# Kernel optimization log

Measured on AMD Instinct MI355X. Metric: run time of the kernel, lower is better.

## Reference

```python
import jax, jax.numpy as jnp
import numpy as np

EPS = 1e-5

def _layernorm(x, g, b):
    m = jnp.mean(x, axis=-1, keepdims=True)
    v = jnp.var(x, axis=-1, keepdims=True)
    return (x - m) * jax.lax.rsqrt(v + EPS) * g + b

def setup_inputs() -> dict:
    key = jax.random.key(0)
    ks = jax.random.split(key, 8)
    B, N, D, H = 4, 2048, 1024, 16
    F = 2 * D
    s = 0.02
    return {
        "x": jax.random.normal(ks[0], (B, N, D), jnp.float32),
        "mask": jnp.zeros((B, N, N), jnp.float32),
        "Wq": jax.random.normal(ks[1], (D, D), jnp.float32) * s,
        "Wk": jax.random.normal(ks[2], (D, D), jnp.float32) * s,
        "Wv": jax.random.normal(ks[3], (D, D), jnp.float32) * s,
        "Wc": jax.random.normal(ks[4], (D, D), jnp.float32) * s,
        "bc": jnp.zeros((D,), jnp.float32),
        "W1": jax.random.normal(ks[5], (D, F), jnp.float32) * s,
        "b1": jnp.zeros((F,), jnp.float32),
        "W2": jax.random.normal(ks[6], (F, D), jnp.float32) * s,
        "b2": jnp.zeros((D,), jnp.float32),
        "g1": jnp.ones((D,), jnp.float32),
        "be1": jnp.zeros((D,), jnp.float32),
        "g2": jnp.ones((D,), jnp.float32),
        "be2": jnp.zeros((D,), jnp.float32),
    }

def reference(x, mask, Wq, Wk, Wv, Wc, bc, W1, b1, W2, b2, g1, be1, g2, be2):
    B, N, D = x.shape
    H = 16
    Dh = D // H
    scale = 1.0 / np.sqrt(Dh).astype(np.float32)
    # projections -> [B, H, N, Dh]
    def heads(t):
        return t.reshape(B, N, H, Dh).transpose(0, 2, 1, 3)
    q = heads(x @ Wq)
    k = heads(x @ Wk)
    v = heads(x @ Wv)
    score = jnp.einsum('bhnd,bhmd->bhnm', q, k) * scale + mask[:, None, :, :]
    attn = jnp.einsum('bhnm,bhmd->bhnd', jax.nn.softmax(score, axis=-1), v)
    attn = attn.transpose(0, 2, 1, 3).reshape(B, N, D)
    x = x + attn @ Wc + bc
    x = _layernorm(x, g1, be1)
    x = x + jnp.maximum(x @ W1 + b1, 0.0) @ W2 + b2
    x = _layernorm(x, g2, be2)
    return x
```

## Files before the change

kernel.cpp:

```cpp
#include <hip/hip_runtime.h>
#include <hip/hip_bf16.h>


#define DEV __device__ __forceinline__

using s16x8  = __attribute__((ext_vector_type(8))) short;
using f32x4  = __attribute__((ext_vector_type(4))) float;

DEV unsigned short f2bf(float f) {
  unsigned u = __float_as_uint(f);
  u += 0x7fffu + ((u >> 16) & 1u);
  return (unsigned short)(u >> 16);
}
DEV unsigned cvt_pk_bf16(float lo, float hi) {
  unsigned r;
  asm("v_cvt_pk_bf16_f32 %0, %1, %2" : "=v"(r) : "v"(lo), "v"(hi));
  return r;
}
DEV float bf2f(unsigned short b) { return __uint_as_float((unsigned)b << 16); }

typedef __attribute__((address_space(3))) unsigned lds_u32_t;
typedef const __attribute__((address_space(1))) unsigned glb_u32_t;

DEV void gld_lds16(const void* g, void* l) {
  __builtin_amdgcn_global_load_lds((glb_u32_t*)g, (lds_u32_t*)l, 16, 0, 0);
}

template<int RELU, int VOUT>
__global__ __launch_bounds__(512, 2)
void gemm8p(const unsigned short* __restrict__ A, const unsigned short* __restrict__ Bt,
            unsigned short* __restrict__ Cb, const float* __restrict__ bias,
            unsigned short* __restrict__ vtout, int M, int N, int K)
{
  __shared__ unsigned short Sh[2][2][256 * 64];
  const int tid = threadIdx.x;
  const int w = tid >> 6, lane = tid & 63;
  const int g = lane >> 4, q = lane & 15;
  const int wr = w >> 2, wc = w & 3;

  const int nwg  = gridDim.x * gridDim.y;
  const int flat = blockIdx.y * gridDim.x + blockIdx.x;
  const int rm   = (flat & 7) * (nwg >> 3) + (flat >> 3);
  const int m0 = (rm / gridDim.x) * 256, n0 = (rm % gridDim.x) * 256;

  f32x4 acc[8][4] = {};

  const int srow = w * 8 + (lane >> 3);
  const int scol = ((lane & 7) ^ (lane >> 3)) * 8;
  const unsigned short* Ag = A  + (size_t)(m0 + srow) * K + scol;
  const unsigned short* Bg = Bt + (size_t)(n0 + srow) * K + scol;

  auto STG = [&](const unsigned short* Gb, int buf, int ab, int half, int kt) {
    const unsigned short* gs = Gb + (size_t)(half * 128) * K + kt * 64;
    unsigned short* ls = &Sh[buf][ab][(half * 128 + w * 8) * 64];
    gld_lds16(gs, ls);
    gld_lds16(gs + (size_t)64 * K, ls + 64 * 64);
  };
  auto LDA = [&](int buf, int mq, s16x8 af[4][2]) {
#pragma unroll
    for (int mm = 0; mm < 4; ++mm) {
      const unsigned short* rp = &Sh[buf][0][(wr * 128 + mq * 64 + mm * 16 + q) * 64];
#pragma unroll
      for (int kk = 0; kk < 2; ++kk)
        af[mm][kk] = *(const s16x8*)(rp + (((kk * 4 + g) ^ (q & 7)) * 8));
    }
  };
  auto LDB = [&](int buf, int nq, s16x8 bf[2][2]) {
#pragma unroll
    for (int nn = 0; nn < 2; ++nn) {
      const unsigned short* rp = &Sh[buf][1][(wc * 64 + nq * 32 + nn * 16 + q) * 64];
#pragma unroll
      for (int kk = 0; kk < 2; ++kk)
        bf[nn][kk] = *(const s16x8*)(rp + (((kk * 4 + g) ^ (q & 7)) * 8));
    }
  };
  auto MQ = [&](int mq, int nq, const s16x8 af[4][2], const s16x8 bf[2][2]) {
    __builtin_amdgcn_s_setprio(1);
#pragma unroll
    for (int kk = 0; kk < 2; ++kk)
#pragma unroll
      for (int mm = 0; mm < 4; ++mm)
#pragma unroll
        for (int nn = 0; nn < 2; ++nn)
          acc[mq * 4 + mm][nq * 2 + nn] = __builtin_amdgcn_mfma_f32_16x16x32_bf16(
              af[mm][kk], bf[nn][kk], acc[mq * 4 + mm][nq * 2 + nn], 0, 0, 0);
    __builtin_amdgcn_s_setprio(0);
  };
  auto BAR = [&]() { __builtin_amdgcn_sched_barrier(0); __builtin_amdgcn_s_barrier(); };

  STG(Ag, 0, 0, 0, 0); STG(Ag, 0, 0, 1, 0);
  STG(Bg, 0, 1, 0, 0); STG(Bg, 0, 1, 1, 0);

  const int NKT = K >> 6;
  s16x8 af[4][2], bf0[2][2], bf1[2][2];
#pragma unroll 1
  for (int kt = 0; kt < NKT; ++kt) {
    const int b = kt & 1, sb = b ^ 1, kn = kt + 1;
    const bool stg = (kn < NKT);
    if (stg) { STG(Ag, sb, 0, 0, kn); asm volatile("s_waitcnt vmcnt(2)" ::: "memory"); }
    else     {                        asm volatile("s_waitcnt vmcnt(0)" ::: "memory"); }
    BAR();
    LDA(b, 0, af); LDB(b, 0, bf0);
    MQ(0, 0, af, bf0);
    BAR();
    if (stg) STG(Ag, sb, 0, 1, kn);
    LDB(b, 1, bf1);
    MQ(0, 1, af, bf1);
    BAR();
    if (stg) STG(Bg, sb, 1, 0, kn);
    LDA(b, 1, af);
    MQ(1, 0, af, bf0);
    BAR();
    if (stg) STG(Bg, sb, 1, 1, kn);
    MQ(1, 1, af, bf1);
    BAR();
  }

#pragma unroll
  for (int n = 0; n < 4; ++n) {
    const int col = n0 + wc * 64 + n * 16 + q;
    if (VOUT && col >= 2048) {
      const int cv = col - 2048;
#pragma unroll
      for (int m = 0; m < 8; ++m) {
        const int row0 = m0 + wr * 128 + m * 16 + g * 4;
        const int bb = row0 >> 11;
        ushort4 pk;
        pk.x = f2bf(acc[m][n][0]); pk.y = f2bf(acc[m][n][1]);
        pk.z = f2bf(acc[m][n][2]); pk.w = f2bf(acc[m][n][3]);
        *(ushort4*)(vtout + ((size_t)bb * 1024 + cv) * 2048 + (row0 & 2047)) = pk;
      }
    } else {
      const float scl = (VOUT && col < 1024) ? 0.18033688011112042f : 1.0f;
      const float bv = bias ? bias[col] : 0.0f;
#pragma unroll
      for (int m = 0; m < 8; ++m) {
        const int row0 = m0 + wr * 128 + m * 16 + g * 4;
#pragma unroll
        for (int r = 0; r < 4; ++r) {
          float v = acc[m][n][r] * scl + bv;
          if (RELU) v = fmaxf(v, 0.0f);
          Cb[(size_t)(row0 + r) * N + col] = f2bf(v);
        }
      }
    }
  }
}

template<int RELU, int RESID, int OUTF>
__global__ __launch_bounds__(256)
void gemm_bt(const unsigned short* __restrict__ A, const unsigned short* __restrict__ Bt,
             unsigned short* __restrict__ Cb, float* __restrict__ Cf,
             const float* __restrict__ bias, const float* __restrict__ resid,
             const unsigned short* __restrict__ residb,
             int M, int N, int K)
{
  __shared__ unsigned short As[2][4096];
  __shared__ unsigned short Bs[2][4096];
  const int tid  = threadIdx.x;
  const int wave = tid >> 6, lane = tid & 63;
  const int g = lane >> 4, q = lane & 15;

  const int nwg  = gridDim.x * gridDim.y;
  const int flat = blockIdx.y * gridDim.x + blockIdx.x;
  const int rm   = (nwg & 7) ? flat : ((flat & 7) * (nwg >> 3) + (flat >> 3));
  const int m0 = (rm / gridDim.x) * 128, n0 = (rm % gridDim.x) * 128;
  const int wr = wave >> 1, wc = wave & 1;

  f32x4 acc[4][4] = {};

  const int i0 = wave * 512 + lane * 8;
  const int i1 = 2048 + i0;

  auto STAGE = [&](int buf, int kt) {
    gld_lds16(A  + (size_t)(m0 + (i0 >> 5)) * K + kt + (i0 & 31), As[buf] + wave * 512);
    gld_lds16(Bt + (size_t)(n0 + (i0 >> 5)) * K + kt + (i0 & 31), Bs[buf] + wave * 512);
    gld_lds16(A  + (size_t)(m0 + (i1 >> 5)) * K + kt + (i1 & 31), As[buf] + 2048 + wave * 512);
    gld_lds16(Bt + (size_t)(n0 + (i1 >> 5)) * K + kt + (i1 & 31), Bs[buf] + 2048 + wave * 512);
  };

  STAGE(0, 0);
  __syncthreads();
  int cur = 0;
#pragma unroll 1
  for (int kt = 0; kt < K; kt += 32) {
    if (kt + 32 < K) STAGE(cur ^ 1, kt + 32);
    s16x8 a[4], b[4];
#pragma unroll
    for (int m = 0; m < 4; ++m)
      a[m] = *(const s16x8*)(As[cur] + (wr * 64 + m * 16 + q) * 32 + g * 8);
#pragma unroll
    for (int n = 0; n < 4; ++n)
      b[n] = *(const s16x8*)(Bs[cur] + (wc * 64 + n * 16 + q) * 32 + g * 8);
    __builtin_amdgcn_s_setprio(1);
#pragma unroll
    for (int m = 0; m < 4; ++m)
#pragma unroll
      for (int n = 0; n < 4; ++n)
        acc[m][n] = __builtin_amdgcn_mfma_f32_16x16x32_bf16(a[m], b[n], acc[m][n], 0, 0, 0);
    __builtin_amdgcn_s_setprio(0);
    __syncthreads();
    cur ^= 1;
  }

#pragma unroll
  for (int n = 0; n < 4; ++n) {
    const int col = n0 + wc * 64 + n * 16 + q;
    const float bv = bias ? bias[col] : 0.0f;
#pragma unroll
    for (int m = 0; m < 4; ++m) {
      const int row0 = m0 + wr * 64 + m * 16 + g * 4;
#pragma unroll
      for (int r = 0; r < 4; ++r) {
        float v = acc[m][n][r] + bv;
        if (RELU) v = fmaxf(v, 0.0f);
        if (RESID == 1) v += resid[(size_t)(row0 + r) * N + col];
        if (RESID == 2) v += bf2f(residb[(size_t)(row0 + r) * N + col]);
        if (OUTF) Cf[(size_t)(row0 + r) * N + col] = v;
        else      Cb[(size_t)(row0 + r) * N + col] = f2bf(v);
      }
    }
  }
}

__global__ __launch_bounds__(256, 4)
void attn_kernel(const unsigned short* __restrict__ qkv,
                 const unsigned short* __restrict__ vt,
                 const float* __restrict__ mask,
                 unsigned short* __restrict__ outb)
{
  __shared__ unsigned short Ks[2][4096];
  __shared__ unsigned short Vs[2][4096];
  __shared__ unsigned short Pl[4][1024];
  const int tid = threadIdx.x, wave = tid >> 6, lane = tid & 63;
  const int g = lane >> 4, q = lane & 15;

  const int flat = blockIdx.y * 32 + blockIdx.x;
  const int rm   = (flat & 7) * 256 + (flat >> 3);
  const int qt = rm & 31, bh = rm >> 5;
  const int b = bh >> 4, h = bh & 15;
  const int qrow = qt * 64 + wave * 16;
  const size_t tok0 = (size_t)b * 2048;

  const unsigned short* Qp = qkv + (tok0 + qrow + q) * 3072 + h * 64;
  const s16x8 bq0 = *(const s16x8*)(Qp + g * 8);
  const s16x8 bq1 = *(const s16x8*)(Qp + 32 + g * 8);
  const float* Mp = mask + ((size_t)b * 2048 + qrow + q) * 2048;

  const int lr = lane >> 3;
  const int sc = (lane & 7) ^ lr;
  const unsigned short* Kg = qkv + tok0 * 3072 + 1024 + h * 64
                           + (size_t)(wave * 16 + lr) * 3072 + sc * 8;
  const unsigned short* Vg = vt + ((size_t)bh * 64 + wave * 16 + lr) * 2048 + sc * 8;
  unsigned short* KsW = Ks[0] + wave * 1024;
  unsigned short* VsW = Vs[0] + wave * 1024;

  auto STAGE = [&](int buf, int t) {
    const size_t ko = (size_t)t * (64 * 3072);
    const int    vo = t * 64;
    gld_lds16(Kg + ko,            KsW + buf * 4096);
    gld_lds16(Kg + ko + 8 * 3072, KsW + buf * 4096 + 512);
    gld_lds16(Vg + vo,            VsW + buf * 4096);
    gld_lds16(Vg + vo + 8 * 2048, VsW + buf * 4096 + 512);
  };

  s16x8 ones;
#pragma unroll
  for (int j = 0; j < 8; ++j) ones[j] = (short)0x3F80;

  f32x4 ot[4] = {};
  f32x4 sacc = {};
  f32x4 mkc[4], mkn[4] = {};
  char* Pw = (char*)&Pl[wave][0];
  const float L2E = 1.4426950408889634f;
  const float MST = -8.0f;

  STAGE(0, 0);
#pragma unroll
  for (int m2 = 0; m2 < 4; ++m2) {
    const f32x4 r = *(const f32x4*)(Mp + m2 * 16 + g * 4);
#pragma unroll
    for (int i = 0; i < 4; ++i) mkc[m2][i] = fmaf(r[i], L2E, MST);
  }
  __syncthreads();

  int cur = 0;
#pragma unroll 1
  for (int t = 0; t < 32; ++t) {
    if (t < 31) {
      STAGE(cur ^ 1, t + 1);
#pragma unroll
      for (int m2 = 0; m2 < 4; ++m2)
        mkn[m2] = *(const f32x4*)(Mp + (t + 1) * 64 + m2 * 16 + g * 4);
    }
    const unsigned short* Kt = Ks[cur];
    const unsigned short* Vt = Vs[cur];

    f32x4 st[4];
#pragma unroll
    for (int m2 = 0; m2 < 4; ++m2) st[m2] = mkc[m2];
    __builtin_amdgcn_s_setprio(1);
#pragma unroll
    for (int m2 = 0; m2 < 4; ++m2) {
      const unsigned short* kp = Kt + (m2 * 16 + q) * 64;
      const s16x8 ak0 = *(const s16x8*)(kp + ((g       ^ (q & 7)) * 8));
      const s16x8 ak1 = *(const s16x8*)(kp + (((g + 4) ^ (q & 7)) * 8));
      st[m2] = __builtin_amdgcn_mfma_f32_16x16x32_bf16(ak0, bq0, st[m2], 0, 0, 0);
      st[m2] = __builtin_amdgcn_mfma_f32_16x16x32_bf16(ak1, bq1, st[m2], 0, 0, 0);
    }
    __builtin_amdgcn_s_setprio(0);

#pragma unroll
    for (int m2 = 0; m2 < 4; ++m2) {
#pragma unroll
      for (int r = 0; r < 4; ++r)
        st[m2][r] = exp2f(st[m2][r]);
      const int bir  = m2 * 32 + g * 8;
      const int addr = q * 128 + (((bir >> 4) ^ (q & 7)) << 4) + (bir & 15);
      uint2 pk;
      pk.x = cvt_pk_bf16(st[m2][0], st[m2][1]);
      pk.y = cvt_pk_bf16(st[m2][2], st[m2][3]);
      *(uint2*)(Pw + addr) = pk;
    }

    __builtin_amdgcn_s_setprio(1);
#pragma unroll
    for (int kb = 0; kb < 2; ++kb) {
      const int blk = (kb * 4 + g) ^ (q & 7);
      const s16x8 pb = *(const s16x8*)(Pw + q * 128 + blk * 16);
      sacc = __builtin_amdgcn_mfma_f32_16x16x32_bf16(ones, pb, sacc, 0, 0, 0);
#pragma unroll
      for (int mm = 0; mm < 4; ++mm) {
        const s16x8 av = *(const s16x8*)(Vt + (mm * 16 + q) * 64 + blk * 8);
        ot[mm] = __builtin_amdgcn_mfma_f32_16x16x32_bf16(av, pb, ot[mm], 0, 0, 0);
      }
    }
    __builtin_amdgcn_s_setprio(0);

#pragma unroll
    for (int m2 = 0; m2 < 4; ++m2)
#pragma unroll
      for (int i = 0; i < 4; ++i) mkc[m2][i] = fmaf(mkn[m2][i], L2E, MST);
    __syncthreads();
    cur ^= 1;
  }

  const float inv = 1.0f / sacc[0];
#pragma unroll
  for (int mm = 0; mm < 4; ++mm) {
    const int bir  = mm * 32 + g * 8;
    const int addr = q * 128 + (((bir >> 4) ^ (q & 7)) << 4) + (bir & 15);
    uint2 pk;
    pk.x = cvt_pk_bf16(ot[mm][0] * inv, ot[mm][1] * inv);
    pk.y = cvt_pk_bf16(ot[mm][2] * inv, ot[mm][3] * inv);
    *(uint2*)(Pw + addr) = pk;
  }
#pragma unroll
  for (int p = 0; p < 2; ++p) {
    const int c  = p * 64 + lane;
    const int qq = c >> 3, cc = c & 7;
    const int blk = cc ^ (qq & 7);
    const s16x8 vv = *(const s16x8*)(Pw + qq * 128 + blk * 16);
    *(s16x8*)(outb + (tok0 + qrow + qq) * 1024 + h * 64 + cc * 8) = vv;
  }
}

template<int INBF>
__global__ __launch_bounds__(256)
void ln_kernel(const float* __restrict__ inf, const unsigned short* __restrict__ inb,
               float* __restrict__ outf, unsigned short* __restrict__ outb,
               const float* __restrict__ gam, const float* __restrict__ bet)
{
  __shared__ float red[8];
  const int row = blockIdx.x, tid = threadIdx.x;
  f32x4 v;
  if (INBF) {
    const uint2 u = *(const uint2*)(inb + (size_t)row * 1024 + tid * 4);
    v[0] = __uint_as_float(u.x << 16); v[1] = __uint_as_float(u.x & 0xffff0000u);
    v[2] = __uint_as_float(u.y << 16); v[3] = __uint_as_float(u.y & 0xffff0000u);
  } else {
    v = *(const f32x4*)(inf + (size_t)row * 1024 + tid * 4);
  }
  float s  = v[0] + v[1] + v[2] + v[3];
  float ss = v[0]*v[0] + v[1]*v[1] + v[2]*v[2] + v[3]*v[3];
#pragma unroll
  for (int o = 1; o < 64; o <<= 1) { s += __shfl_xor(s, o); ss += __shfl_xor(ss, o); }
  if ((tid & 63) == 0) { red[tid >> 6] = s; red[4 + (tid >> 6)] = ss; }
  __syncthreads();
  s  = red[0] + red[1] + red[2] + red[3];
  ss = red[4] + red[5] + red[6] + red[7];
  const float mean = s * (1.0f / 1024.0f);
  const float var  = ss * (1.0f / 1024.0f) - mean * mean;
  const float rstd = rsqrtf(var + 1e-5f);
  const f32x4 gm = *(const f32x4*)(gam + tid * 4);
  const f32x4 bt = *(const f32x4*)(bet + tid * 4);
  f32x4 o;
#pragma unroll
  for (int j = 0; j < 4; ++j) o[j] = (v[j] - mean) * rstd * gm[j] + bt[j];
  if (outf) *(f32x4*)(outf + (size_t)row * 1024 + tid * 4) = o;
  if (outb) {
    uint2 pk; pk.x = cvt_pk_bf16(o[0], o[1]); pk.y = cvt_pk_bf16(o[2], o[3]);
    *(uint2*)(outb + (size_t)row * 1024 + tid * 4) = pk;
  }
}

__global__ __launch_bounds__(256)
void tcast_kernel(const float* __restrict__ in, unsigned short* __restrict__ out, int R, int C)
{
  __shared__ float t[32][33];
  const int tx = threadIdx.x & 31, ty = threadIdx.x >> 5;
  const int c0 = blockIdx.x * 32, r0 = blockIdx.y * 32;
#pragma unroll
  for (int k = 0; k < 4; ++k)
    t[ty + k * 8][tx] = in[(size_t)(r0 + ty + k * 8) * C + c0 + tx];
  __syncthreads();
#pragma unroll
  for (int k = 0; k < 4; ++k)
    out[(size_t)(c0 + ty + k * 8) * R + r0 + tx] = f2bf(t[tx][ty + k * 8]);
}

__global__ __launch_bounds__(256)
void cast_x_kernel(const float* __restrict__ in, unsigned short* __restrict__ out)
{
  const size_t i = ((size_t)blockIdx.x * 256 + threadIdx.x) * 4;
  const f32x4 v = *(const f32x4*)(in + i);
  uint2 pk; pk.x = cvt_pk_bf16(v[0], v[1]); pk.y = cvt_pk_bf16(v[2], v[3]);
  *(uint2*)(out + i) = pk;
}

extern "C" void kernel_launch(void* const* d_in, const int* in_sizes, int n_in,
                              void* d_out, int out_size, void* d_ws, size_t ws_size,
                              hipStream_t stream)
{
  (void)in_sizes; (void)n_in; (void)out_size; (void)ws_size;
  const float* x   = (const float*)d_in[0];
  const float* msk = (const float*)d_in[1];
  const float* Wq  = (const float*)d_in[2];
  const float* Wk  = (const float*)d_in[3];
  const float* Wv  = (const float*)d_in[4];
  const float* Wc  = (const float*)d_in[5];
  const float* bc  = (const float*)d_in[6];
  const float* W1  = (const float*)d_in[7];
  const float* b1  = (const float*)d_in[8];
  const float* W2  = (const float*)d_in[9];
  const float* b2  = (const float*)d_in[10];
  const float* g1  = (const float*)d_in[11];
  const float* be1 = (const float*)d_in[12];
  const float* g2  = (const float*)d_in[13];
  const float* be2 = (const float*)d_in[14];
  float* out = (float*)d_out;
  char* ws = (char*)d_ws;
  const size_t MB = 1u << 20;
  unsigned short* xb    = (unsigned short*)(ws + 0 * MB);
  unsigned short* wqkvt = (unsigned short*)(ws + 16 * MB);
  unsigned short* wct   = (unsigned short*)(ws + 22 * MB);
  unsigned short* w1t   = (unsigned short*)(ws + 24 * MB);
  unsigned short* w2t   = (unsigned short*)(ws + 28 * MB);
  unsigned short* qkv   = (unsigned short*)(ws + 32 * MB);
  unsigned short* vt    = (unsigned short*)(ws + 80 * MB);
  unsigned short* attnb = (unsigned short*)(ws + 96 * MB);
  unsigned short* y1b   = (unsigned short*)(ws + 112 * MB);
  unsigned short* midb  = (unsigned short*)(ws + 32 * MB);
  unsigned short* z2b   = (unsigned short*)(ws + 64 * MB);
  unsigned short* h1b   = (unsigned short*)(ws + 128 * MB);

  cast_x_kernel<<<8192, 256, 0, stream>>>(x, xb);
  tcast_kernel<<<dim3(32, 32), 256, 0, stream>>>(Wq, wqkvt,               1024, 1024);
  tcast_kernel<<<dim3(32, 32), 256, 0, stream>>>(Wk, wqkvt + 1024 * 1024, 1024, 1024);
  tcast_kernel<<<dim3(32, 32), 256, 0, stream>>>(Wv, wqkvt + 2048 * 1024, 1024, 1024);
  tcast_kernel<<<dim3(32, 32), 256, 0, stream>>>(Wc, wct,                 1024, 1024);
  tcast_kernel<<<dim3(64, 32), 256, 0, stream>>>(W1, w1t,                 1024, 2048);
  tcast_kernel<<<dim3(32, 64), 256, 0, stream>>>(W2, w2t,                 2048, 1024);

  gemm8p<0, 1><<<dim3(12, 32), 512, 0, stream>>>(xb, wqkvt, qkv, nullptr, vt,
                                                 8192, 3072, 1024);
  attn_kernel<<<dim3(32, 64), 256, 0, stream>>>(qkv, vt, msk, attnb);
  gemm_bt<0, 2, 0><<<dim3(8, 64), 256, 0, stream>>>(attnb, wct, y1b, nullptr,
                                                    bc, nullptr, xb, 8192, 1024, 1024);
  ln_kernel<1><<<8192, 256, 0, stream>>>(nullptr, y1b, nullptr, h1b, g1, be1);
  gemm8p<1, 0><<<dim3(8, 32), 512, 0, stream>>>(h1b, w1t, midb, b1, nullptr,
                                                8192, 2048, 1024);
  gemm_bt<0, 2, 0><<<dim3(8, 64), 256, 0, stream>>>(midb, w2t, z2b, nullptr,
                                                    b2, nullptr, h1b, 8192, 1024, 2048);
  ln_kernel<1><<<8192, 256, 0, stream>>>(nullptr, z2b, out, nullptr, g2, be2);
}
```

Before: 420.0 us.

## Precast mask to bf16, unroll attention tile loop, move QKV GEMM to 128-tile kernel

Adds a kernel that turns the fp32 mask into bf16 pre-scaled by log2(e) with the -8 offset, so attention reads half the mask bytes and skips the per-tile FMA. The attention loop is unrolled by two with a macro so buffer indices and mask registers become compile-time fixed. The QKV projection moves from the 256x256 gemm8p kernel to the 128x128 gemm_bt kernel, which gains the V-transpose output path. Risks include an extra full pass over the 64MB mask, bf16 precision loss in the mask, and a smaller tile GEMM for QKV.

```diff
diff --git a/kernel.cpp b/kernel.cpp
--- a/kernel.cpp
+++ b/kernel.cpp
@@ -26,11 +26,11 @@
   __builtin_amdgcn_global_load_lds((glb_u32_t*)g, (lds_u32_t*)l, 16, 0, 0);
 }
 
-template<int RELU, int VOUT>
+template<int RELU>
 __global__ __launch_bounds__(512, 2)
 void gemm8p(const unsigned short* __restrict__ A, const unsigned short* __restrict__ Bt,
             unsigned short* __restrict__ Cb, const float* __restrict__ bias,
-            unsigned short* __restrict__ vtout, int M, int N, int K)
+            int M, int N, int K)
 {
   __shared__ unsigned short Sh[2][2][256 * 64];
   const int tid = threadIdx.x;
@@ -119,11 +119,85 @@
 #pragma unroll
   for (int n = 0; n < 4; ++n) {
     const int col = n0 + wc * 64 + n * 16 + q;
+    const float bv = bias ? bias[col] : 0.0f;
+#pragma unroll
+    for (int m = 0; m < 8; ++m) {
+      const int row0 = m0 + wr * 128 + m * 16 + g * 4;
+#pragma unroll
+      for (int r = 0; r < 4; ++r) {
+        float v = acc[m][n][r] + bv;
+        if (RELU) v = fmaxf(v, 0.0f);
+        Cb[(size_t)(row0 + r) * N + col] = f2bf(v);
+      }
+    }
+  }
+}
+
+template<int RELU, int RESID, int OUTF, int VOUT>
+__global__ __launch_bounds__(256)
+void gemm_bt(const unsigned short* __restrict__ A, const unsigned short* __restrict__ Bt,
+             unsigned short* __restrict__ Cb, float* __restrict__ Cf,
+             const float* __restrict__ bias, const float* __restrict__ resid,
+             const unsigned short* __restrict__ residb,
+             unsigned short* __restrict__ vtout,
+             int M, int N, int K)
+{
+  __shared__ unsigned short As[2][4096];
+  __shared__ unsigned short Bs[2][4096];
+  const int tid  = threadIdx.x;
+  const int wave = tid >> 6, lane = tid & 63;
+  const int g = lane >> 4, q = lane & 15;
+
+  const int nwg  = gridDim.x * gridDim.y;
+  const int flat = blockIdx.y * gridDim.x + blockIdx.x;
+  const int rm   = (nwg & 7) ? flat : ((flat & 7) * (nwg >> 3) + (flat >> 3));
+  const int m0 = (rm / gridDim.x) * 128, n0 = (rm % gridDim.x) * 128;
+  const int wr = wave >> 1, wc = wave & 1;
+
+  f32x4 acc[4][4] = {};
+
+  const int i0 = wave * 512 + lane * 8;
+  const int i1 = 2048 + i0;
+
+  auto STAGE = [&](int buf, int kt) {
+    gld_lds16(A  + (size_t)(m0 + (i0 >> 5)) * K + kt + (i0 & 31), As[buf] + wave * 512);
+    gld_lds16(Bt + (size_t)(n0 + (i0 >> 5)) * K + kt + (i0 & 31), Bs[buf] + wave * 512);
+    gld_lds16(A  + (size_t)(m0 + (i1 >> 5)) * K + kt + (i1 & 31), As[buf] + 2048 + wave * 512);
+    gld_lds16(Bt + (size_t)(n0 + (i1 >> 5)) * K + kt + (i1 & 31), Bs[buf] + 2048 + wave * 512);
+  };
+
+  STAGE(0, 0);
+  __syncthreads();
+  int cur = 0;
+#pragma unroll 1
+  for (int kt = 0; kt < K; kt += 32) {
+    if (kt + 32 < K) STAGE(cur ^ 1, kt + 32);
+    s16x8 a[4], b[4];
+#pragma unroll
+    for (int m = 0; m < 4; ++m)
+      a[m] = *(const s16x8*)(As[cur] + (wr * 64 + m * 16 + q) * 32 + g * 8);
+#pragma unroll
+    for (int n = 0; n < 4; ++n)
+      b[n] = *(const s16x8*)(Bs[cur] + (wc * 64 + n * 16 + q) * 32 + g * 8);
+    __builtin_amdgcn_s_setprio(1);
+#pragma unroll
+    for (int m = 0; m < 4; ++m)
+#pragma unroll
+      for (int n = 0; n < 4; ++n)
+        acc[m][n] = __builtin_amdgcn_mfma_f32_16x16x32_bf16(a[m], b[n], acc[m][n], 0, 0, 0);
+    __builtin_amdgcn_s_setprio(0);
+    __syncthreads();
+    cur ^= 1;
+  }
+
+#pragma unroll
+  for (int n = 0; n < 4; ++n) {
+    const int col = n0 + wc * 64 + n * 16 + q;
     if (VOUT && col >= 2048) {
       const int cv = col - 2048;
 #pragma unroll
-      for (int m = 0; m < 8; ++m) {
-        const int row0 = m0 + wr * 128 + m * 16 + g * 4;
+      for (int m = 0; m < 4; ++m) {
+        const int row0 = m0 + wr * 64 + m * 16 + g * 4;
         const int bb = row0 >> 11;
         ushort4 pk;
         pk.x = f2bf(acc[m][n][0]); pk.y = f2bf(acc[m][n][1]);
@@ -134,99 +208,38 @@
       const float scl = (VOUT && col < 1024) ? 0.18033688011112042f : 1.0f;
       const float bv = bias ? bias[col] : 0.0f;
 #pragma unroll
-      for (int m = 0; m < 8; ++m) {
-        const int row0 = m0 + wr * 128 + m * 16 + g * 4;
+      for (int m = 0; m < 4; ++m) {
+        const int row0 = m0 + wr * 64 + m * 16 + g * 4;
 #pragma unroll
         for (int r = 0; r < 4; ++r) {
-          float v = acc[m][n][r] * scl + bv;
+          float v = VOUT ? (acc[m][n][r] * scl) : (acc[m][n][r] + bv);
           if (RELU) v = fmaxf(v, 0.0f);
-          Cb[(size_t)(row0 + r) * N + col] = f2bf(v);
+          if (RESID == 1) v += resid[(size_t)(row0 + r) * N + col];
+          if (RESID == 2) v += bf2f(residb[(size_t)(row0 + r) * N + col]);
+          if (OUTF) Cf[(size_t)(row0 + r) * N + col] = v;
+          else      Cb[(size_t)(row0 + r) * N + col] = f2bf(v);
         }
       }
     }
   }
 }
 
-template<int RELU, int RESID, int OUTF>
 __global__ __launch_bounds__(256)
-void gemm_bt(const unsigned short* __restrict__ A, const unsigned short* __restrict__ Bt,
-             unsigned short* __restrict__ Cb, float* __restrict__ Cf,
-             const float* __restrict__ bias, const float* __restrict__ resid,
-             const unsigned short* __restrict__ residb,
-             int M, int N, int K)
-{
-  __shared__ unsigned short As[2][4096];
-  __shared__ unsigned short Bs[2][4096];
-  const int tid  = threadIdx.x;
-  const int wave = tid >> 6, lane = tid & 63;
-  const int g = lane >> 4, q = lane & 15;
-
-  const int nwg  = gridDim.x * gridDim.y;
-  const int flat = blockIdx.y * gridDim.x + blockIdx.x;
-  const int rm   = (nwg & 7) ? flat : ((flat & 7) * (nwg >> 3) + (flat >> 3));
-  const int m0 = (rm / gridDim.x) * 128, n0 = (rm % gridDim.x) * 128;
-  const int wr = wave >> 1, wc = wave & 1;
-
-  f32x4 acc[4][4] = {};
-
-  const int i0 = wave * 512 + lane * 8;
-  const int i1 = 2048 + i0;
-
-  auto STAGE = [&](int buf, int kt) {
-    gld_lds16(A  + (size_t)(m0 + (i0 >> 5)) * K + kt + (i0 & 31), As[buf] + wave * 512);
-    gld_lds16(Bt + (size_t)(n0 + (i0 >> 5)) * K + kt + (i0 & 31), Bs[buf] + wave * 512);
-    gld_lds16(A  + (size_t)(m0 + (i1 >> 5)) * K + kt + (i1 & 31), As[buf] + 2048 + wave * 512);
-    gld_lds16(Bt + (size_t)(n0 + (i1 >> 5)) * K + kt + (i1 & 31), Bs[buf] + 2048 + wave * 512);
-  };
-
-  STAGE(0, 0);
-  __syncthreads();
-  int cur = 0;
-#pragma unroll 1
-  for (int kt = 0; kt < K; kt += 32) {
-    if (kt + 32 < K) STAGE(cur ^ 1, kt + 32);
-    s16x8 a[4], b[4];
-#pragma unroll
-    for (int m = 0; m < 4; ++m)
-      a[m] = *(const s16x8*)(As[cur] + (wr * 64 + m * 16 + q) * 32 + g * 8);
-#pragma unroll
-    for (int n = 0; n < 4; ++n)
-      b[n] = *(const s16x8*)(Bs[cur] + (wc * 64 + n * 16 + q) * 32 + g * 8);
-    __builtin_amdgcn_s_setprio(1);
-#pragma unroll
-    for (int m = 0; m < 4; ++m)
-#pragma unroll
-      for (int n = 0; n < 4; ++n)
-        acc[m][n] = __builtin_amdgcn_mfma_f32_16x16x32_bf16(a[m], b[n], acc[m][n], 0, 0, 0);
-    __builtin_amdgcn_s_setprio(0);
-    __syncthreads();
-    cur ^= 1;
-  }
-
-#pragma unroll
-  for (int n = 0; n < 4; ++n) {
-    const int col = n0 + wc * 64 + n * 16 + q;
-    const float bv = bias ? bias[col] : 0.0f;
-#pragma unroll
-    for (int m = 0; m < 4; ++m) {
-      const int row0 = m0 + wr * 64 + m * 16 + g * 4;
-#pragma unroll
-      for (int r = 0; r < 4; ++r) {
-        float v = acc[m][n][r] + bv;
-        if (RELU) v = fmaxf(v, 0.0f);
-        if (RESID == 1) v += resid[(size_t)(row0 + r) * N + col];
-        if (RESID == 2) v += bf2f(residb[(size_t)(row0 + r) * N + col]);
-        if (OUTF) Cf[(size_t)(row0 + r) * N + col] = v;
-        else      Cb[(size_t)(row0 + r) * N + col] = f2bf(v);
-      }
-    }
-  }
+void mcast_kernel(const float* __restrict__ in, unsigned short* __restrict__ out)
+{
+  const size_t i = ((size_t)blockIdx.x * 256 + threadIdx.x) * 4;
+  const f32x4 v = *(const f32x4*)(in + i);
+  const float L2E = 1.4426950408889634f;
+  uint2 pk;
+  pk.x = cvt_pk_bf16(fmaf(v[0], L2E, -8.0f), fmaf(v[1], L2E, -8.0f));
+  pk.y = cvt_pk_bf16(fmaf(v[2], L2E, -8.0f), fmaf(v[3], L2E, -8.0f));
+  *(uint2*)(out + i) = pk;
 }
 
 __global__ __launch_bounds__(256, 4)
 void attn_kernel(const unsigned short* __restrict__ qkv,
                  const unsigned short* __restrict__ vt,
-                 const float* __restrict__ mask,
+                 const unsigned short* __restrict__ mkb,
                  unsigned short* __restrict__ outb)
 {
   __shared__ unsigned short Ks[2][4096];
@@ -245,7 +258,7 @@
   const unsigned short* Qp = qkv + (tok0 + qrow + q) * 3072 + h * 64;
   const s16x8 bq0 = *(const s16x8*)(Qp + g * 8);
   const s16x8 bq1 = *(const s16x8*)(Qp + 32 + g * 8);
-  const float* Mp = mask + ((size_t)b * 2048 + qrow + q) * 2048;
+  const unsigned short* Mb = mkb + ((size_t)b * 2048 + qrow + q) * 2048 + g * 4;
 
   const int lr = lane >> 3;
   const int sc = (lane & 7) ^ lr;
@@ -255,95 +268,96 @@
   unsigned short* KsW = Ks[0] + wave * 1024;
   unsigned short* VsW = Vs[0] + wave * 1024;
 
-  auto STAGE = [&](int buf, int t) {
-    const size_t ko = (size_t)t * (64 * 3072);
-    const int    vo = t * 64;
-    gld_lds16(Kg + ko,            KsW + buf * 4096);
-    gld_lds16(Kg + ko + 8 * 3072, KsW + buf * 4096 + 512);
-    gld_lds16(Vg + vo,            VsW + buf * 4096);
-    gld_lds16(Vg + vo + 8 * 2048, VsW + buf * 4096 + 512);
-  };
-
   s16x8 ones;
 #pragma unroll
   for (int j = 0; j < 8; ++j) ones[j] = (short)0x3F80;
 
   f32x4 ot[4] = {};
   f32x4 sacc = {};
-  f32x4 mkc[4], mkn[4] = {};
+  f32x4 mk0[4], mk1[4];
   char* Pw = (char*)&Pl[wave][0];
-  const float L2E = 1.4426950408889634f;
-  const float MST = -8.0f;
-
-  STAGE(0, 0);
+
+  gld_lds16(Kg,            KsW);
+  gld_lds16(Kg + 8 * 3072, KsW + 512);
+  gld_lds16(Vg,            VsW);
+  gld_lds16(Vg + 8 * 2048, VsW + 512);
 #pragma unroll
   for (int m2 = 0; m2 < 4; ++m2) {
-    const f32x4 r = *(const f32x4*)(Mp + m2 * 16 + g * 4);
-#pragma unroll
-    for (int i = 0; i < 4; ++i) mkc[m2][i] = fmaf(r[i], L2E, MST);
+    const uint2 u = *(const uint2*)(Mb + m2 * 16);
+    mk0[m2][0] = __uint_as_float(u.x << 16);
+    mk0[m2][1] = __uint_as_float(u.x & 0xffff0000u);
+    mk0[m2][2] = __uint_as_float(u.y << 16);
+    mk0[m2][3] = __uint_as_float(u.y & 0xffff0000u);
   }
   __syncthreads();
 
-  int cur = 0;
+#define ATTN_TILE(BUF, MKC, MKN, STG)                                          \
+  {                                                                            \
+    uint2 mu[4];                                                               \
+    if (STG) {                                                                 \
+      Kg += 64 * 3072; Vg += 64; Mb += 64;                                     \
+      gld_lds16(Kg,            KsW + (BUF ^ 1) * 4096);                        \
+      gld_lds16(Kg + 8 * 3072, KsW + (BUF ^ 1) * 4096 + 512);                  \
+      gld_lds16(Vg,            VsW + (BUF ^ 1) * 4096);                        \
+      gld_lds16(Vg + 8 * 2048, VsW + (BUF ^ 1) * 4096 + 512);                  \
+      mu[0] = *(const uint2*)(Mb);      mu[1] = *(const uint2*)(Mb + 16);      \
+      mu[2] = *(const uint2*)(Mb + 32); mu[3] = *(const uint2*)(Mb + 48);      \
+    }                                                                          \
+    f32x4 st[4];                                                               \
+    _Pragma("unroll")                                                          \
+    for (int m2 = 0; m2 < 4; ++m2) st[m2] = MKC[m2];                           \
+    __builtin_amdgcn_s_setprio(1);                                             \
+    _Pragma("unroll")                                                          \
+    for (int m2 = 0; m2 < 4; ++m2) {                                           \
+      const unsigned short* kp = Ks[BUF] + (m2 * 16 + q) * 64;                 \
+      const s16x8 ak0 = *(const s16x8*)(kp + ((g       ^ (q & 7)) * 8));       \
+      const s16x8 ak1 = *(const s16x8*)(kp + (((g + 4) ^ (q & 7)) * 8));       \
+      st[m2] = __builtin_amdgcn_mfma_f32_16x16x32_bf16(ak0, bq0, st[m2], 0, 0, 0); \
+      st[m2] = __builtin_amdgcn_mfma_f32_16x16x32_bf16(ak1, bq1, st[m2], 0, 0, 0); \
+    }                                                                          \
+    __builtin_amdgcn_s_setprio(0);                                             \
+    _Pragma("unroll")                                                          \
+    for (int m2 = 0; m2 < 4; ++m2) {                                           \
+      st[m2][0] = exp2f(st[m2][0]); st[m2][1] = exp2f(st[m2][1]);              \
+      st[m2][2] = exp2f(st[m2][2]); st[m2][3] = exp2f(st[m2][3]);              \
+      const int bir  = m2 * 32 + g * 8;                                        \
+      const int addr = q * 128 + (((bir >> 4) ^ (q & 7)) << 4) + (bir & 15);   \
+      uint2 pk;                                                                \
+      pk.x = cvt_pk_bf16(st[m2][0], st[m2][1]);                                \
+      pk.y = cvt_pk_bf16(st[m2][2], st[m2][3]);                                \
+      *(uint2*)(Pw + addr) = pk;                                               \
+    }                                                                          \
+    __builtin_amdgcn_s_setprio(1);                                             \
+    _Pragma("unroll")                                                          \
+    for (int kb = 0; kb < 2; ++kb) {                                           \
+      const int blk = (kb * 4 + g) ^ (q & 7);                                  \
+      const s16x8 pb = *(const s16x8*)(Pw + q * 128 + blk * 16);               \
+      sacc = __builtin_amdgcn_mfma_f32_16x16x32_bf16(ones, pb, sacc, 0, 0, 0); \
+      _Pragma("unroll")                                                        \
+      for (int mm = 0; mm < 4; ++mm) {                                         \
+        const s16x8 av = *(const s16x8*)(Vs[BUF] + (mm * 16 + q) * 64 + blk * 8); \
+        ot[mm] = __builtin_amdgcn_mfma_f32_16x16x32_bf16(av, pb, ot[mm], 0, 0, 0); \
+      }                                                                        \
+    }                                                                          \
+    __builtin_amdgcn_s_setprio(0);                                             \
+    if (STG) {                                                                 \
+      _Pragma("unroll")                                                        \
+      for (int m2 = 0; m2 < 4; ++m2) {                                         \
+        MKN[m2][0] = __uint_as_float(mu[m2].x << 16);                          \
+        MKN[m2][1] = __uint_as_float(mu[m2].x & 0xffff0000u);                  \
+        MKN[m2][2] = __uint_as_float(mu[m2].y << 16);                          \
+        MKN[m2][3] = __uint_as_float(mu[m2].y & 0xffff0000u);                  \
+      }                                                                        \
+    }                                                                          \
+    __syncthreads();                                                           \
+  }
+
 #pragma unroll 1
-  for (int t = 0; t < 32; ++t) {
-    if (t < 31) {
-      STAGE(cur ^ 1, t + 1);
-#pragma unroll
-      for (int m2 = 0; m2 < 4; ++m2)
-        mkn[m2] = *(const f32x4*)(Mp + (t + 1) * 64 + m2 * 16 + g * 4);
-    }
-    const unsigned short* Kt = Ks[cur];
-    const unsigned short* Vt = Vs[cur];
-
-    f32x4 st[4];
-#pragma unroll
-    for (int m2 = 0; m2 < 4; ++m2) st[m2] = mkc[m2];
-    __builtin_amdgcn_s_setprio(1);
-#pragma unroll
-    for (int m2 = 0; m2 < 4; ++m2) {
-      const unsigned short* kp = Kt + (m2 * 16 + q) * 64;
-      const s16x8 ak0 = *(const s16x8*)(kp + ((g       ^ (q & 7)) * 8));
-      const s16x8 ak1 = *(const s16x8*)(kp + (((g + 4) ^ (q & 7)) * 8));
-      st[m2] = __builtin_amdgcn_mfma_f32_16x16x32_bf16(ak0, bq0, st[m2], 0, 0, 0);
-      st[m2] = __builtin_amdgcn_mfma_f32_16x16x32_bf16(ak1, bq1, st[m2], 0, 0, 0);
-    }
-    __builtin_amdgcn_s_setprio(0);
-
-#pragma unroll
-    for (int m2 = 0; m2 < 4; ++m2) {
-#pragma unroll
-      for (int r = 0; r < 4; ++r)
-        st[m2][r] = exp2f(st[m2][r]);
-      const int bir  = m2 * 32 + g * 8;
-      const int addr = q * 128 + (((bir >> 4) ^ (q & 7)) << 4) + (bir & 15);
-      uint2 pk;
-      pk.x = cvt_pk_bf16(st[m2][0], st[m2][1]);
-      pk.y = cvt_pk_bf16(st[m2][2], st[m2][3]);
-      *(uint2*)(Pw + addr) = pk;
-    }
-
-    __builtin_amdgcn_s_setprio(1);
-#pragma unroll
-    for (int kb = 0; kb < 2; ++kb) {
-      const int blk = (kb * 4 + g) ^ (q & 7);
-      const s16x8 pb = *(const s16x8*)(Pw + q * 128 + blk * 16);
-      sacc = __builtin_amdgcn_mfma_f32_16x16x32_bf16(ones, pb, sacc, 0, 0, 0);
-#pragma unroll
-      for (int mm = 0; mm < 4; ++mm) {
-        const s16x8 av = *(const s16x8*)(Vt + (mm * 16 + q) * 64 + blk * 8);
-        ot[mm] = __builtin_amdgcn_mfma_f32_16x16x32_bf16(av, pb, ot[mm], 0, 0, 0);
-      }
-    }
-    __builtin_amdgcn_s_setprio(0);
-
-#pragma unroll
-    for (int m2 = 0; m2 < 4; ++m2)
-#pragma unroll
-      for (int i = 0; i < 4; ++i) mkc[m2][i] = fmaf(mkn[m2][i], L2E, MST);
-    __syncthreads();
-    cur ^= 1;
-  }
+  for (int tt = 0; tt < 16; ++tt) {
+    ATTN_TILE(0, mk0, mk1, true);
+    ATTN_TILE(1, mk1, mk0, (tt < 15));
+  }
+#undef ATTN_TILE
 
   const float inv = 1.0f / sacc[0];
 #pragma unroll
@@ -459,12 +473,14 @@
   unsigned short* qkv   = (unsigned short*)(ws + 32 * MB);
   unsigned short* vt    = (unsigned short*)(ws + 80 * MB);
   unsigned short* attnb = (unsigned short*)(ws + 96 * MB);
+  unsigned short* mkb   = (unsigned short*)(ws + 112 * MB);
   unsigned short* y1b   = (unsigned short*)(ws + 112 * MB);
+  unsigned short* h1b   = (unsigned short*)(ws + 128 * MB);
   unsigned short* midb  = (unsigned short*)(ws + 32 * MB);
   unsigned short* z2b   = (unsigned short*)(ws + 64 * MB);
-  unsigned short* h1b   = (unsigned short*)(ws + 128 * MB);
 
   cast_x_kernel<<<8192, 256, 0, stream>>>(x, xb);
+  mcast_kernel<<<16384, 256, 0, stream>>>(msk, mkb);
   tcast_kernel<<<dim3(32, 32), 256, 0, stream>>>(Wq, wqkvt,               1024, 1024);
   tcast_kernel<<<dim3(32, 32), 256, 0, stream>>>(Wk, wqkvt + 1024 * 1024, 1024, 1024);
   tcast_kernel<<<dim3(32, 32), 256, 0, stream>>>(Wv, wqkvt + 2048 * 1024, 1024, 1024);
@@ -472,15 +488,17 @@
   tcast_kernel<<<dim3(64, 32), 256, 0, stream>>>(W1, w1t,                 1024, 2048);
   tcast_kernel<<<dim3(32, 64), 256, 0, stream>>>(W2, w2t,                 2048, 1024);
 
-  gemm8p<0, 1><<<dim3(12, 32), 512, 0, stream>>>(xb, wqkvt, qkv, nullptr, vt,
-                                                 8192, 3072, 1024);
-  attn_kernel<<<dim3(32, 64), 256, 0, stream>>>(qkv, vt, msk, attnb);
-  gemm_bt<0, 2, 0><<<dim3(8, 64), 256, 0, stream>>>(attnb, wct, y1b, nullptr,
-                                                    bc, nullptr, xb, 8192, 1024, 1024);
+  gemm_bt<0, 0, 0, 1><<<dim3(24, 64), 256, 0, stream>>>(xb, wqkvt, qkv, nullptr,
+                                                        nullptr, nullptr, nullptr, vt,
+                                                        8192, 3072, 1024);
+  attn_kernel<<<dim3(32, 64), 256, 0, stream>>>(qkv, vt, mkb, attnb);
+  gemm_bt<0, 2, 0, 0><<<dim3(8, 64), 256, 0, stream>>>(attnb, wct, y1b, nullptr,
+                                                       bc, nullptr, xb, nullptr,
+                                                       8192, 1024, 1024);
   ln_kernel<1><<<8192, 256, 0, stream>>>(nullptr, y1b, nullptr, h1b, g1, be1);
-  gemm8p<1, 0><<<dim3(8, 32), 512, 0, stream>>>(h1b, w1t, midb, b1, nullptr,
-                                                8192, 2048, 1024);
-  gemm_bt<0, 2, 0><<<dim3(8, 64), 256, 0, stream>>>(midb, w2t, z2b, nullptr,
-                                                    b2, nullptr, h1b, 8192, 1024, 2048);
+  gemm8p<1><<<dim3(8, 32), 512, 0, stream>>>(h1b, w1t, midb, b1, 8192, 2048, 1024);
+  gemm_bt<0, 2, 0, 0><<<dim3(8, 64), 256, 0, stream>>>(midb, w2t, z2b, nullptr,
+                                                       b2, nullptr, h1b, nullptr,
+                                                       8192, 1024, 2048);
   ln_kernel<1><<<8192, 256, 0, stream>>>(nullptr, z2b, out, nullptr, g2, be2);
 }
```

Measured after the change: 422.4 us. About the same (+0.6%).
